# Kernel optimization log

Hardware: AMD Instinct MI355X
Metric: run time of the kernel (lower is better)

The kernel has to match this reference:

```python
import jax, jax.numpy as jnp
import numpy as np

QMIN, QMAX, QLEVELS = -128, 127, 127.0


def setup_inputs() -> dict:
    key = jax.random.key(0)
    k1, k2, k3 = jax.random.split(key, 3)
    x = jax.random.normal(k1, (128, 1024), dtype=jnp.float32)          # [tokens, in]
    weight = jax.random.normal(k2, (1024, 1024), dtype=jnp.float32) * 0.02  # [out, in]
    bias = jax.random.normal(k3, (1024,), dtype=jnp.float32) * 0.01
    # LUT of (approximate) int8 products; exact products used as reference baseline.
    q = jnp.arange(QMIN, QMAX + 1, dtype=jnp.float32)                  # [256]
    lut = q[:, None] * q[None, :]                                      # [256, 256]
    T_feature = jnp.float32(4.0)   # EMA-tracked activation absmax threshold
    T_weight = jnp.float32(0.12)   # EMA-tracked weight absmax threshold
    return {"x": x, "weight": weight, "bias": bias, "lut": lut,
            "T_feature": T_feature, "T_weight": T_weight}


def reference(x, weight, bias, lut, T_feature, T_weight):
    # EMA threshold update (update_T=True path in the torch module)
    Tf = 0.95 * T_feature + 0.05 * jnp.max(jnp.abs(x))
    Tw = 0.95 * T_weight + 0.05 * jnp.max(jnp.abs(weight))
    sx = Tf / QLEVELS
    sw = Tw / QLEVELS
    # symmetric int8 quantization against the EMA thresholds
    qx = jnp.clip(jnp.round(x / sx), QMIN, QMAX).astype(jnp.int32)       # [T, K]
    qw = jnp.clip(jnp.round(weight / sw), QMIN, QMAX).astype(jnp.int32)  # [N, K]
    # LUT-based dequant matmul: sum_k lut[qx[t,k]+128, qw[n,k]+128]
    lut_flat = lut.reshape(-1)                                           # [65536]
    idx = (qx + 128)[:, None, :] * 256 + (qw + 128)[None, :, :]          # [T, N, K]
    acc = jnp.take(lut_flat, idx).sum(axis=-1)                           # [T, N]
    out = acc * (sx * sw) + bias
    return out
```

## Files before the change

kernel.cpp:

```cpp
#include <hip/hip_runtime.h>

typedef int v4i __attribute__((ext_vector_type(4)));

__global__ __launch_bounds__(256) void absmax_partial(
    const float* __restrict__ x, const float* __restrict__ w,
    float2* __restrict__ partials) {
  int tid = threadIdx.x;
  int gtid = blockIdx.x * 256 + tid;
  float mx = 0.f, mw = 0.f;
  const float4* x4 = (const float4*)x;
  const float4* w4 = (const float4*)w;
  for (int i = gtid; i < 32768; i += 65536) {
    float4 v = x4[i];
    mx = fmaxf(mx, fmaxf(fmaxf(fabsf(v.x), fabsf(v.y)),
                         fmaxf(fabsf(v.z), fabsf(v.w))));
  }
  #pragma unroll
  for (int it = 0; it < 4; ++it) {
    float4 v = w4[gtid + it * 65536];
    mw = fmaxf(mw, fmaxf(fmaxf(fabsf(v.x), fabsf(v.y)),
                         fmaxf(fabsf(v.z), fabsf(v.w))));
  }
  #pragma unroll
  for (int off = 32; off; off >>= 1) {
    mx = fmaxf(mx, __shfl_xor(mx, off));
    mw = fmaxf(mw, __shfl_xor(mw, off));
  }
  __shared__ float smx[4], smw[4];
  int wid = tid >> 6;
  if ((tid & 63) == 0) { smx[wid] = mx; smw[wid] = mw; }
  __syncthreads();
  if (tid == 0) {
    partials[blockIdx.x] =
        make_float2(fmaxf(fmaxf(smx[0], smx[1]), fmaxf(smx[2], smx[3])),
                    fmaxf(fmaxf(smw[0], smw[1]), fmaxf(smw[2], smw[3])));
  }
}

__device__ __forceinline__ void wave_scales(const float2* partials, int lane,
                                            const float* Tf, const float* Tw,
                                            float& sx, float& sw,
                                            float& inv_sx, float& inv_sw) {
  float pm = 0.f, pw = 0.f;
  #pragma unroll
  for (int it = 0; it < 4; ++it) {
    float2 p = partials[lane + it * 64];
    pm = fmaxf(pm, p.x);
    pw = fmaxf(pw, p.y);
  }
  #pragma unroll
  for (int off = 32; off; off >>= 1) {
    pm = fmaxf(pm, __shfl_xor(pm, off));
    pw = fmaxf(pw, __shfl_xor(pw, off));
  }
  float TfN = 0.95f * Tf[0] + 0.05f * pm;
  float TwN = 0.95f * Tw[0] + 0.05f * pw;
  sx = TfN * (1.0f / 127.0f);
  sw = TwN * (1.0f / 127.0f);
  inv_sx = 127.0f / TfN;
  inv_sw = 127.0f / TwN;
}

__device__ __forceinline__ int packq(float4 v, float inv) {
  float t0 = fminf(fmaxf(rintf(v.x * inv), -128.f), 127.f);
  float t1 = fminf(fmaxf(rintf(v.y * inv), -128.f), 127.f);
  float t2 = fminf(fmaxf(rintf(v.z * inv), -128.f), 127.f);
  float t3 = fminf(fmaxf(rintf(v.w * inv), -128.f), 127.f);
  int q0 = (int)t0, q1 = (int)t1, q2 = (int)t2, q3 = (int)t3;
  return (q0 & 255) | ((q1 & 255) << 8) | ((q2 & 255) << 16) | (q3 << 24);
}

__global__ __launch_bounds__(256) void quant_kernel(
    const float* __restrict__ x, const float* __restrict__ w,
    const float2* __restrict__ partials,
    const float* __restrict__ Tf, const float* __restrict__ Tw,
    int* __restrict__ qxi, int* __restrict__ qwi) {
  int tid = threadIdx.x;
  int lane = tid & 63;
  float sx, sw, inv_sx, inv_sw;
  wave_scales(partials, lane, Tf, Tw, sx, sw, inv_sx, inv_sw);

  int gtid = blockIdx.x * 256 + tid;
  const float4* x4 = (const float4*)x;
  const float4* w4 = (const float4*)w;
  for (int i = gtid; i < 32768; i += 65536)
    qxi[i] = packq(x4[i], inv_sx);
  #pragma unroll
  for (int it = 0; it < 4; ++it) {
    int i = gtid + it * 65536;
    qwi[i] = packq(w4[i], inv_sw);
  }
}

__global__ __launch_bounds__(256) void gemm_kernel(
    const char* __restrict__ qx, const char* __restrict__ qw,
    const float2* __restrict__ partials,
    const float* __restrict__ Tf, const float* __restrict__ Tw,
    const float* __restrict__ bias, float* __restrict__ out) {
  int tid = threadIdx.x;
  int lane = tid & 63;
  int wid = tid >> 6;

  float sx, sw, inv_sx, inv_sw;
  wave_scales(partials, lane, Tf, Tw, sx, sw, inv_sx, inv_sw);

  int nt  = blockIdx.x & 63;
  int mtp = blockIdx.x >> 6;

  int arow0 = (mtp << 5) + (lane & 15);
  int brow  = (nt << 4) + (lane & 15);
  int kidx  = (lane >> 4) + (wid << 4);

  const v4i* a0 = (const v4i*)qx + arow0 * 64 + kidx;
  const v4i* a1 = a0 + 1024;
  const v4i* b4 = (const v4i*)qw + brow * 64 + kidx;

  v4i acc0 = {0, 0, 0, 0}, acc1 = {0, 0, 0, 0};
  #pragma unroll
  for (int kk = 0; kk < 4; ++kk) {
    v4i a = a0[kk * 4];
    v4i c = a1[kk * 4];
    v4i b = b4[kk * 4];
    acc0 = __builtin_amdgcn_mfma_i32_16x16x64_i8(a, b, acc0, 0, 0, 0);
    acc1 = __builtin_amdgcn_mfma_i32_16x16x64_i8(c, b, acc1, 0, 0, 0);
  }

  __shared__ v4i comb[4][2][64];
  comb[wid][0][lane] = acc0;
  comb[wid][1][lane] = acc1;
  __syncthreads();

  if (wid < 2) {
    v4i s0 = comb[0][wid][lane];
    v4i s1 = comb[1][wid][lane];
    v4i s2 = comb[2][wid][lane];
    v4i s3 = comb[3][wid][lane];
    int mt = (mtp << 1) + wid;
    int orow = (mt << 4) + ((lane >> 4) << 2);
    int col  = (nt << 4) + (lane & 15);
    float bcol = bias[col];
    float s = sx * sw;
    #pragma unroll
    for (int r = 0; r < 4; ++r) {
      out[(orow + r) * 1024 + col] =
          (float)(s0[r] + s1[r] + s2[r] + s3[r]) * s + bcol;
    }
  }
}

extern "C" void kernel_launch(void* const* d_in, const int* in_sizes, int n_in,
                              void* d_out, int out_size, void* d_ws, size_t ws_size,
                              hipStream_t stream) {
  const float* x    = (const float*)d_in[0];
  const float* w    = (const float*)d_in[1];
  const float* bias = (const float*)d_in[2];
  const float* Tf   = (const float*)d_in[4];
  const float* Tw   = (const float*)d_in[5];
  float* out = (float*)d_out;

  float2* partials = (float2*)d_ws;
  char* qx = (char*)d_ws + 4096;
  char* qw = qx + 128 * 1024;

  absmax_partial<<<256, 256, 0, stream>>>(x, w, partials);
  quant_kernel<<<256, 256, 0, stream>>>(x, w, partials, Tf, Tw,
                                        (int*)qx, (int*)qw);
  gemm_kernel<<<256, 256, 0, stream>>>(qx, qw, partials, Tf, Tw, bias, out);
}
```

Before: 15.85 us.

## Double grid for absmax/quant kernels and pass precomputed scale to GEMM

Raises the absmax and quantization kernels from 256 to 512 blocks, so each thread handles two weight float4s instead of four and at most one activation float4. The quant kernel now reduces 512 partials and writes the combined dequant scale to workspace. The GEMM reads that single float instead of re-reducing the partials in every block. This trades more blocks and a larger partial reduction for more memory-level parallelism and less redundant work in the GEMM prologue.

```diff
diff --git a/kernel.cpp b/kernel.cpp
--- a/kernel.cpp
+++ b/kernel.cpp
@@ -10,14 +10,13 @@
   float mx = 0.f, mw = 0.f;
   const float4* x4 = (const float4*)x;
   const float4* w4 = (const float4*)w;
-  for (int i = gtid; i < 32768; i += 65536) {
-    float4 v = x4[i];
-    mx = fmaxf(mx, fmaxf(fmaxf(fabsf(v.x), fabsf(v.y)),
-                         fmaxf(fabsf(v.z), fabsf(v.w))));
+  if (gtid < 32768) {
+    float4 v = x4[gtid];
+    mx = fmaxf(fmaxf(fabsf(v.x), fabsf(v.y)), fmaxf(fabsf(v.z), fabsf(v.w)));
   }
   #pragma unroll
-  for (int it = 0; it < 4; ++it) {
-    float4 v = w4[gtid + it * 65536];
+  for (int it = 0; it < 2; ++it) {
+    float4 v = w4[gtid + it * 131072];
     mw = fmaxf(mw, fmaxf(fmaxf(fabsf(v.x), fabsf(v.y)),
                          fmaxf(fabsf(v.z), fabsf(v.w))));
   }
@@ -37,30 +36,6 @@
   }
 }
 
-__device__ __forceinline__ void wave_scales(const float2* partials, int lane,
-                                            const float* Tf, const float* Tw,
-                                            float& sx, float& sw,
-                                            float& inv_sx, float& inv_sw) {
-  float pm = 0.f, pw = 0.f;
-  #pragma unroll
-  for (int it = 0; it < 4; ++it) {
-    float2 p = partials[lane + it * 64];
-    pm = fmaxf(pm, p.x);
-    pw = fmaxf(pw, p.y);
-  }
-  #pragma unroll
-  for (int off = 32; off; off >>= 1) {
-    pm = fmaxf(pm, __shfl_xor(pm, off));
-    pw = fmaxf(pw, __shfl_xor(pw, off));
-  }
-  float TfN = 0.95f * Tf[0] + 0.05f * pm;
-  float TwN = 0.95f * Tw[0] + 0.05f * pw;
-  sx = TfN * (1.0f / 127.0f);
-  sw = TwN * (1.0f / 127.0f);
-  inv_sx = 127.0f / TfN;
-  inv_sw = 127.0f / TwN;
-}
-
 __device__ __forceinline__ int packq(float4 v, float inv) {
   float t0 = fminf(fmaxf(rintf(v.x * inv), -128.f), 127.f);
   float t1 = fminf(fmaxf(rintf(v.y * inv), -128.f), 127.f);
@@ -74,35 +49,50 @@
     const float* __restrict__ x, const float* __restrict__ w,
     const float2* __restrict__ partials,
     const float* __restrict__ Tf, const float* __restrict__ Tw,
-    int* __restrict__ qxi, int* __restrict__ qwi) {
+    int* __restrict__ qxi, int* __restrict__ qwi,
+    float* __restrict__ scale_out) {
   int tid = threadIdx.x;
   int lane = tid & 63;
-  float sx, sw, inv_sx, inv_sw;
-  wave_scales(partials, lane, Tf, Tw, sx, sw, inv_sx, inv_sw);
+
+  float pm = 0.f, pw = 0.f;
+  #pragma unroll
+  for (int it = 0; it < 8; ++it) {
+    float2 p = partials[lane + it * 64];
+    pm = fmaxf(pm, p.x);
+    pw = fmaxf(pw, p.y);
+  }
+  #pragma unroll
+  for (int off = 32; off; off >>= 1) {
+    pm = fmaxf(pm, __shfl_xor(pm, off));
+    pw = fmaxf(pw, __shfl_xor(pw, off));
+  }
+  float TfN = 0.95f * Tf[0] + 0.05f * pm;
+  float TwN = 0.95f * Tw[0] + 0.05f * pw;
+  float inv_sx = 127.0f / TfN;
+  float inv_sw = 127.0f / TwN;
+
+  if (blockIdx.x == 0 && tid == 0)
+    scale_out[0] = (TfN * (1.0f / 127.0f)) * (TwN * (1.0f / 127.0f));
 
   int gtid = blockIdx.x * 256 + tid;
   const float4* x4 = (const float4*)x;
   const float4* w4 = (const float4*)w;
-  for (int i = gtid; i < 32768; i += 65536)
-    qxi[i] = packq(x4[i], inv_sx);
+  if (gtid < 32768)
+    qxi[gtid] = packq(x4[gtid], inv_sx);
   #pragma unroll
-  for (int it = 0; it < 4; ++it) {
-    int i = gtid + it * 65536;
+  for (int it = 0; it < 2; ++it) {
+    int i = gtid + it * 131072;
     qwi[i] = packq(w4[i], inv_sw);
   }
 }
 
 __global__ __launch_bounds__(256) void gemm_kernel(
     const char* __restrict__ qx, const char* __restrict__ qw,
-    const float2* __restrict__ partials,
-    const float* __restrict__ Tf, const float* __restrict__ Tw,
+    const float* __restrict__ scale_in,
     const float* __restrict__ bias, float* __restrict__ out) {
   int tid = threadIdx.x;
   int lane = tid & 63;
   int wid = tid >> 6;
-
-  float sx, sw, inv_sx, inv_sw;
-  wave_scales(partials, lane, Tf, Tw, sx, sw, inv_sx, inv_sw);
 
   int nt  = blockIdx.x & 63;
   int mtp = blockIdx.x >> 6;
@@ -139,7 +129,7 @@
     int orow = (mt << 4) + ((lane >> 4) << 2);
     int col  = (nt << 4) + (lane & 15);
     float bcol = bias[col];
-    float s = sx * sw;
+    float s = scale_in[0];
     #pragma unroll
     for (int r = 0; r < 4; ++r) {
       out[(orow + r) * 1024 + col] =
@@ -159,11 +149,12 @@
   float* out = (float*)d_out;
 
   float2* partials = (float2*)d_ws;
-  char* qx = (char*)d_ws + 4096;
+  float*  scales   = (float*)((char*)d_ws + 4096);
+  char* qx = (char*)d_ws + 8192;
   char* qw = qx + 128 * 1024;
 
-  absmax_partial<<<256, 256, 0, stream>>>(x, w, partials);
-  quant_kernel<<<256, 256, 0, stream>>>(x, w, partials, Tf, Tw,
-                                        (int*)qx, (int*)qw);
-  gemm_kernel<<<256, 256, 0, stream>>>(qx, qw, partials, Tf, Tw, bias, out);
+  absmax_partial<<<512, 256, 0, stream>>>(x, w, partials);
+  quant_kernel<<<512, 256, 0, stream>>>(x, w, partials, Tf, Tw,
+                                        (int*)qx, (int*)qw, scales);
+  gemm_kernel<<<256, 256, 0, stream>>>(qx, qw, scales, bias, out);
 }
```

New measurement: 15.87 us. About the same (+0.1%).
